# Optimization experiments

Hardware: AMD Instinct MI355X
Metric: run time of the kernel (lower is better)

Reference implementation:

```python
import jax, jax.numpy as jnp
import numpy as np
from jax import lax

R = 128            # grid resolution (full-depth N3Tree equivalent)
BASIS = 9          # SH degree 2 -> 9 basis functions
DATA_DIM = 3 * BASIS + 1
B = 262144         # rays (512x512 image)
STEP_SIZE = 0.001
BG = 1.0           # background_brightness
NUM_STEPS = 256    # >= sqrt(3)*R worst-case voxel crossings

SH_C0 = 0.28209479177387814
SH_C1 = 0.4886025119029199
SH_C2 = (1.0925484305920792, -1.0925484305920792, 0.31539156525252005,
         -1.0925484305920792, 0.5462742152960396)


def eval_sh_bases(d):
    # d: [B,3] unit view directions -> [B,9] SH deg-2 basis values (matches svox.sh)
    x, y, z = d[:, 0], d[:, 1], d[:, 2]
    return jnp.stack([
        jnp.full_like(x, SH_C0),
        -SH_C1 * y,
        SH_C1 * z,
        -SH_C1 * x,
        SH_C2[0] * x * y,
        SH_C2[1] * y * z,
        SH_C2[2] * (2.0 * z * z - x * x - y * y),
        SH_C2[3] * x * z,
        SH_C2[4] * (x * x - y * y),
    ], axis=-1)


def dda_unit(cen, invdir):
    # slab intersection of ray (cen + t*dir) with unit cube [0,1]^3
    t1 = -cen * invdir            # [B,3]
    t2 = t1 + invdir
    tmin = jnp.maximum(jnp.max(jnp.minimum(t1, t2), axis=-1), 0.0)
    tmax = jnp.minimum(jnp.min(jnp.maximum(t1, t2), axis=-1), 1e9)
    return tmin, tmax


def setup_inputs() -> dict:
    key = jax.random.key(0)
    k1, k2, k3, k4 = jax.random.split(key, 4)
    origins = jax.random.uniform(k1, (B, 3), jnp.float32, 0.05, 0.95)
    dirs = jax.random.normal(k2, (B, 3), jnp.float32)
    viewdirs = jax.random.normal(k3, (B, 3), jnp.float32)
    viewdirs = viewdirs / jnp.linalg.norm(viewdirs, axis=-1, keepdims=True)
    tree_data = jax.random.normal(k4, (R, R, R, DATA_DIM), jnp.float32) * 0.5
    invradius = jnp.ones((3,), jnp.float32)
    return {"tree_data": tree_data, "origins": origins, "dirs": dirs,
            "viewdirs": viewdirs, "invradius": invradius}


def _render(tree_data, origins, dirs, viewdirs, invradius):
    nb = origins.shape[0]
    dirs = dirs / jnp.linalg.norm(dirs, axis=-1, keepdims=True)
    sh_mult = eval_sh_bases(viewdirs)[:, None, :]          # [B,1,9]
    invdirs = 1.0 / (dirs + 1e-9)
    t0, tmax = dda_unit(origins, invdirs)
    delta_scale = jnp.linalg.norm(dirs / invradius[None], axis=-1)  # [B]
    grid = tree_data.reshape(R * R * R, DATA_DIM)
    cube_sz = 1.0 / R

    def step(carry, _):
        t, light, out, active = carry
        pos = origins + t[:, None] * dirs                  # [B,3] in tree coords
        idx = jnp.clip(jnp.floor(pos * R), 0.0, R - 1.0)
        flat = (idx[:, 0] * (R * R) + idx[:, 1] * R + idx[:, 2]).astype(jnp.int32)
        rgba = grid[flat]                                  # [B,28] voxel query
        pos_t = pos * R - idx                              # local coords in voxel
        s0, s1 = dda_unit(pos_t, invdirs)
        dt = (s1 - s0) * cube_sz + STEP_SIZE
        sigma = jax.nn.relu(rgba[:, -1])
        att = jnp.exp(-dt * sigma * delta_scale)
        weight = light * (1.0 - att)
        rgb_sh = rgba[:, :-1].reshape(-1, 3, BASIS)
        rgb = jax.nn.sigmoid(jnp.sum(sh_mult * rgb_sh, axis=-1))  # [B,3]
        am = active[:, None]
        out = out + jnp.where(am, weight[:, None] * rgb, 0.0)
        light = jnp.where(active, light * att, light)
        t = t + jnp.where(active, dt, 0.0)
        active = active & (t < tmax)
        return (t, light, out, active), None

    init = (t0, jnp.ones((nb,), jnp.float32), jnp.zeros((nb, 3), jnp.float32),
            t0 < tmax)
    (t, light, out, active), _ = lax.scan(step, init, None, length=NUM_STEPS)
    # remaining transmittance hits background (white by default)
    return out + light[:, None] * BG


def reference(tree_data, origins, dirs, viewdirs, invradius):
    return _render(tree_data, origins, dirs, viewdirs, invradius)
```

## Files before the change

### kernel.cpp

```cpp
#include <hip/hip_runtime.h>
#include <hip/hip_fp16.h>
#include <math.h>

#define GRID_R 128
#define DATA_DIM 28
#define PAD_DIM 32
#define NSEG 8
#define SEG_STEPS 32
#define STEP_SIZE 0.001f
#define BG 1.0f

typedef _Float16 h2f __attribute__((ext_vector_type(2)));

#if __has_builtin(__builtin_amdgcn_fdot2)
__device__ __forceinline__ float fdot2(h2f a, h2f b, float c) {
    return __builtin_amdgcn_fdot2(a, b, c, false);
}
#else
__device__ __forceinline__ float fdot2(h2f a, h2f b, float c) {
    return fmaf((float)a.x, (float)b.x, fmaf((float)a.y, (float)b.y, c));
}
#endif

#if __has_builtin(__builtin_amdgcn_exp2f)
__device__ __forceinline__ float fexp2(float x)    { return __builtin_amdgcn_exp2f(x); }
__device__ __forceinline__ float fexp2neg(float x) { return __builtin_amdgcn_exp2f(-x); }
#else
__device__ __forceinline__ float fexp2(float x) {
    float r; asm("v_exp_f32 %0, %1" : "=v"(r) : "v"(x)); return r;
}
__device__ __forceinline__ float fexp2neg(float x) {
    float r; asm("v_exp_f32 %0, -%1" : "=v"(r) : "v"(x)); return r;
}
#endif

#if __has_builtin(__builtin_amdgcn_rcpf)
__device__ __forceinline__ float frcp(float x) { return __builtin_amdgcn_rcpf(x); }
#else
__device__ __forceinline__ float frcp(float x) {
    float r; asm("v_rcp_f32 %0, %1" : "=v"(r) : "v"(x)); return r;
}
#endif

__device__ __forceinline__ float march_step(
    float t, float ox, float oy, float oz,
    float dx, float dy, float dz,
    float idx, float idy, float idz, int* flat)
{
    float px = (ox + t*dx) * 128.0f;
    float py = (oy + t*dy) * 128.0f;
    float pz = (oz + t*dz) * 128.0f;
    float fx = fminf(fmaxf(floorf(px), 0.0f), 127.0f);
    float fy = fminf(fmaxf(floorf(py), 0.0f), 127.0f);
    float fz = fminf(fmaxf(floorf(pz), 0.0f), 127.0f);
    float ff = fmaf(fx, 16384.0f, fmaf(fy, 128.0f, fz));
    *flat = (int)ff;
    float cx = px - fx, cy = py - fy, cz = pz - fz;
    float a1x = -cx*idx, a1y = -cy*idy, a1z = -cz*idz;
    float a2x = a1x+idx, a2y = a1y+idy, a2z = a1z+idz;
    float e1 = fminf(fminf(fmaxf(a1x,a2x), fmaxf(a1y,a2y)), fmaxf(a1z,a2z));
    e1 = fminf(e1, 1e9f);
    return e1 * (1.0f/128.0f) + STEP_SIZE;
}

#define RAY_SETUP(i)                                                          \
    float ox = origins[3*(i)+0], oy = origins[3*(i)+1], oz = origins[3*(i)+2];\
    float dx = dirs_in[3*(i)+0], dy = dirs_in[3*(i)+1], dz = dirs_in[3*(i)+2];\
    float dn = sqrtf(dx*dx + dy*dy + dz*dz);                                  \
    float rdn = 1.0f / dn;                                                    \
    dx *= rdn; dy *= rdn; dz *= rdn;                                          \
    float idx = 1.0f / (dx + 1e-9f);                                          \
    float idy = 1.0f / (dy + 1e-9f);                                          \
    float idz = 1.0f / (dz + 1e-9f);                                          \
    float t1x = -ox*idx, t1y = -oy*idy, t1z = -oz*idz;                        \
    float t2x = t1x+idx, t2y = t1y+idy, t2z = t1z+idz;                        \
    float t0   = fmaxf(fmaxf(fmaxf(fminf(t1x,t2x), fminf(t1y,t2y)), fminf(t1z,t2z)), 0.0f); \
    float tmax = fminf(fminf(fminf(fmaxf(t1x,t2x), fmaxf(t1y,t2y)), fmaxf(t1z,t2z)), 1e9f);

__global__ __launch_bounds__(256) void prep_kernel(
    const float* __restrict__ tree, __half* __restrict__ vox, int nvox,
    const float* __restrict__ origins, const float* __restrict__ dirs_in,
    float* __restrict__ ckpt, int nB, int nGeomB)
{
    if ((int)blockIdx.x < nGeomB) {
        int i = blockIdx.x * 256 + threadIdx.x;
        if (i >= nB) return;
        RAY_SETUP(i);
        float ck[NSEG];
        float t = t0;
        ck[0] = t0;
#pragma unroll
        for (int k = 1; k < NSEG; ++k) {
            if (t < tmax) {
                for (int j = 0; j < SEG_STEPS; ++j) {
                    int fl;
                    t += march_step(t, ox, oy, oz, dx, dy, dz, idx, idy, idz, &fl);
                    if (t >= tmax) break;
                }
            }
            ck[k] = t;
        }
        float* cp = ckpt + (size_t)i * NSEG;
        *(float4*)(cp + 0) = make_float4(ck[0], ck[1], ck[2], ck[3]);
        *(float4*)(cp + 4) = make_float4(ck[4], ck[5], ck[6], ck[7]);
    } else {
        int v = (blockIdx.x - nGeomB) * 256 + threadIdx.x;
        if (v >= nvox) return;
        const float4* s4 = (const float4*)(tree + (size_t)v * DATA_DIM);
        float4 A  = s4[0], B4 = s4[1], C4 = s4[2], D4 = s4[3],
               E4 = s4[4], F4 = s4[5], G4 = s4[6];
        uint4* d = (uint4*)(vox + (size_t)v * PAD_DIM);
        union Q { __half2 h[4]; uint4 u; } q;
        q.h[0] = __floats2half2_rn(A.x,  A.y);
        q.h[1] = __floats2half2_rn(A.z,  A.w);
        q.h[2] = __floats2half2_rn(B4.x, B4.y);
        q.h[3] = __floats2half2_rn(B4.z, B4.w);
        d[0] = q.u;
        q.h[0] = __floats2half2_rn(C4.x, 0.f);
        q.h[1] = __floats2half2_rn(C4.y, C4.z);
        q.h[2] = __floats2half2_rn(C4.w, D4.x);
        q.h[3] = __floats2half2_rn(D4.y, D4.z);
        d[1] = q.u;
        q.h[0] = __floats2half2_rn(D4.w, E4.x);
        q.h[1] = __floats2half2_rn(E4.y, 0.f);
        q.h[2] = __floats2half2_rn(E4.z, E4.w);
        q.h[3] = __floats2half2_rn(F4.x, F4.y);
        d[2] = q.u;
        q.h[0] = __floats2half2_rn(F4.z, F4.w);
        q.h[1] = __floats2half2_rn(G4.x, G4.y);
        q.h[2] = __floats2half2_rn(G4.z, 0.f);
        q.h[3] = __floats2half2_rn(G4.w, 0.f);
        d[3] = q.u;
    }
}

__global__ __launch_bounds__(256, 8) void march_kernel(
    const __half* __restrict__ vox_grid,
    const float* __restrict__ origins,
    const float* __restrict__ dirs_in,
    const float* __restrict__ viewdirs,
    const float* __restrict__ invradius,
    const float* __restrict__ ckpt,
    float* __restrict__ out, int nB)
{
    int tid = blockIdx.x * blockDim.x + threadIdx.x;
    int ray = tid >> 3;
    int seg = tid & 7;
    if (ray >= nB) return;

    RAY_SETUP(ray);

    float vx = viewdirs[3*ray+0], vy = viewdirs[3*ray+1], vz = viewdirs[3*ray+2];
    float irx = invradius[0], iry = invradius[1], irz = invradius[2];
    float qx = dx / irx, qy = dy / iry, qz = dz / irz;
    float delta_scale = sqrtf(qx*qx + qy*qy + qz*qz);

    const float C1 = 0.4886025119029199f;
    const float L2E = 1.4426950408889634f;
    float sh0 = 0.28209479177387814f;
    float sh1 = -C1 * vy;
    float sh2 =  C1 * vz;
    float sh3 = -C1 * vx;
    float sh4 =  1.0925484305920792f  * vx * vy;
    float sh5 = -1.0925484305920792f * vy * vz;
    float sh6 =  0.31539156525252005f * (2.0f*vz*vz - vx*vx - vy*vy);
    float sh7 = -1.0925484305920792f * vx * vz;
    float sh8 =  0.5462742152960396f  * (vx*vx - vy*vy);

    h2f S01 = { (_Float16)(sh0*L2E), (_Float16)(sh1*L2E) };
    h2f S23 = { (_Float16)(sh2*L2E), (_Float16)(sh3*L2E) };
    h2f S45 = { (_Float16)(sh4*L2E), (_Float16)(sh5*L2E) };
    h2f S67 = { (_Float16)(sh6*L2E), (_Float16)(sh7*L2E) };
    h2f S8z = { (_Float16)(sh8*L2E), (_Float16)0.0f      };
    float nds = -delta_scale * L2E;

    float t = ckpt[(size_t)ray * NSEG + seg];
    float light = 1.0f;
    float o0 = 0.f, o1 = 0.f, o2 = 0.f;

    for (int j = 0; j < SEG_STEPS; ++j) {
        if (t >= tmax) break;
        int flat;
        float dt = march_step(t, ox, oy, oz, dx, dy, dz, idx, idy, idz, &flat);

        const uint4* vp = (const uint4*)(vox_grid + (size_t)flat * PAD_DIM);
        union { uint4 u[4]; h2f h[16]; _Float16 s[32]; } rec;
        rec.u[0] = vp[0]; rec.u[1] = vp[1]; rec.u[2] = vp[2]; rec.u[3] = vp[3];

        float sigma = fmaxf((float)rec.s[30], 0.0f);
        float att = fexp2(dt * sigma * nds);
        float la  = light * att;
        float w   = light - la;
        light = la;

        float r0 = fdot2(rec.h[ 4], S8z, fdot2(rec.h[ 3], S67, fdot2(rec.h[ 2], S45,
                   fdot2(rec.h[ 1], S23, fdot2(rec.h[ 0], S01, 0.0f)))));
        float r1 = fdot2(rec.h[ 9], S8z, fdot2(rec.h[ 8], S67, fdot2(rec.h[ 7], S45,
                   fdot2(rec.h[ 6], S23, fdot2(rec.h[ 5], S01, 0.0f)))));
        float r2 = fdot2(rec.h[14], S8z, fdot2(rec.h[13], S67, fdot2(rec.h[12], S45,
                   fdot2(rec.h[11], S23, fdot2(rec.h[10], S01, 0.0f)))));

        float g0 = frcp(1.0f + fexp2neg(r0));
        float g1 = frcp(1.0f + fexp2neg(r1));
        float g2 = frcp(1.0f + fexp2neg(r2));

        o0 = fmaf(w, g0, o0);
        o1 = fmaf(w, g1, o1);
        o2 = fmaf(w, g2, o2);

        t += dt;
    }

    float l0 = __shfl(light, 0, 8);
    float l1 = __shfl(light, 1, 8);
    float l2 = __shfl(light, 2, 8);
    float l3 = __shfl(light, 3, 8);
    float l4 = __shfl(light, 4, 8);
    float l5 = __shfl(light, 5, 8);
    float l6 = __shfl(light, 6, 8);
    float l7 = __shfl(light, 7, 8);

    float P = 1.0f;
    if (seg > 0) P *= l0;
    if (seg > 1) P *= l1;
    if (seg > 2) P *= l2;
    if (seg > 3) P *= l3;
    if (seg > 4) P *= l4;
    if (seg > 5) P *= l5;
    if (seg > 6) P *= l6;
    float total_light = l0*l1*l2*l3*l4*l5*l6*l7;

    o0 *= P; o1 *= P; o2 *= P;
    o0 += __shfl_xor(o0, 1, 8); o0 += __shfl_xor(o0, 2, 8); o0 += __shfl_xor(o0, 4, 8);
    o1 += __shfl_xor(o1, 1, 8); o1 += __shfl_xor(o1, 2, 8); o1 += __shfl_xor(o1, 4, 8);
    o2 += __shfl_xor(o2, 1, 8); o2 += __shfl_xor(o2, 2, 8); o2 += __shfl_xor(o2, 4, 8);

    if (seg == 0) {
        out[3*ray+0] = o0 + total_light * BG;
        out[3*ray+1] = o1 + total_light * BG;
        out[3*ray+2] = o2 + total_light * BG;
    }
}

extern "C" void kernel_launch(void* const* d_in, const int* in_sizes, int n_in,
                              void* d_out, int out_size, void* d_ws, size_t ws_size,
                              hipStream_t stream) {
    const float* tree      = (const float*)d_in[0];
    const float* origins   = (const float*)d_in[1];
    const float* dirs      = (const float*)d_in[2];
    const float* viewdirs  = (const float*)d_in[3];
    const float* invradius = (const float*)d_in[4];
    float* out = (float*)d_out;

    int nB   = in_sizes[1] / 3;
    int nvox = in_sizes[0] / DATA_DIM;

    const int block = 256;
    __half* hgrid = (__half*)d_ws;
    float* ckpt = (float*)((char*)d_ws + (size_t)nvox * PAD_DIM * sizeof(__half));

    int nGeomB = (nB + block - 1) / block;
    int nConvB = (nvox + block - 1) / block;
    prep_kernel<<<nGeomB + nConvB, block, 0, stream>>>(
        tree, hgrid, nvox, origins, dirs, ckpt, nB, nGeomB);

    int nmarch = nB * NSEG;
    march_kernel<<<(nmarch + block - 1) / block, block, 0, stream>>>(
        hgrid, origins, dirs, viewdirs, invradius, ckpt, out, nB);
    (void)ws_size;
}
```

Before: 680.5 us.

## Software-pipeline voxel loads in march loop and split grid conversion across two threads

The march loop now computes the next step's voxel index and issues its 64-byte record load before shading the current voxel, double-buffering the two records so gather latency overlaps with SH and exp math. Separately, the fp32 to fp16 grid conversion uses two threads per voxel, each writing half of the padded record. The prefetch can load one extra voxel past the segment end and raises register pressure under launch bounds of 8 waves per SIMD. The conversion split doubles the thread count for that phase.

Result: slower. 706.4 us (+3.8%).

```diff
diff --git a/kernel.cpp b/kernel.cpp
--- a/kernel.cpp
+++ b/kernel.cpp
@@ -104,35 +104,72 @@
         *(float4*)(cp + 0) = make_float4(ck[0], ck[1], ck[2], ck[3]);
         *(float4*)(cp + 4) = make_float4(ck[4], ck[5], ck[6], ck[7]);
     } else {
-        int v = (blockIdx.x - nGeomB) * 256 + threadIdx.x;
+        int tid2 = (blockIdx.x - nGeomB) * 256 + threadIdx.x;
+        int v = tid2 >> 1;
+        int q = tid2 & 1;
         if (v >= nvox) return;
-        const float4* s4 = (const float4*)(tree + (size_t)v * DATA_DIM);
-        float4 A  = s4[0], B4 = s4[1], C4 = s4[2], D4 = s4[3],
-               E4 = s4[4], F4 = s4[5], G4 = s4[6];
-        uint4* d = (uint4*)(vox + (size_t)v * PAD_DIM);
-        union Q { __half2 h[4]; uint4 u; } q;
-        q.h[0] = __floats2half2_rn(A.x,  A.y);
-        q.h[1] = __floats2half2_rn(A.z,  A.w);
-        q.h[2] = __floats2half2_rn(B4.x, B4.y);
-        q.h[3] = __floats2half2_rn(B4.z, B4.w);
-        d[0] = q.u;
-        q.h[0] = __floats2half2_rn(C4.x, 0.f);
-        q.h[1] = __floats2half2_rn(C4.y, C4.z);
-        q.h[2] = __floats2half2_rn(C4.w, D4.x);
-        q.h[3] = __floats2half2_rn(D4.y, D4.z);
-        d[1] = q.u;
-        q.h[0] = __floats2half2_rn(D4.w, E4.x);
-        q.h[1] = __floats2half2_rn(E4.y, 0.f);
-        q.h[2] = __floats2half2_rn(E4.z, E4.w);
-        q.h[3] = __floats2half2_rn(F4.x, F4.y);
-        d[2] = q.u;
-        q.h[0] = __floats2half2_rn(F4.z, F4.w);
-        q.h[1] = __floats2half2_rn(G4.x, G4.y);
-        q.h[2] = __floats2half2_rn(G4.z, 0.f);
-        q.h[3] = __floats2half2_rn(G4.w, 0.f);
-        d[3] = q.u;
+        const float* src = tree + (size_t)v * DATA_DIM;
+        uint4* d = (uint4*)(vox + (size_t)v * PAD_DIM) + q * 2;
+        union Q { __half2 h[4]; uint4 u; } w;
+        if (q == 0) {
+            float4 L0 = *(const float4*)(src + 0);
+            float4 L1 = *(const float4*)(src + 4);
+            float4 L2 = *(const float4*)(src + 8);
+            float4 L3 = *(const float4*)(src + 12);
+            w.h[0] = __floats2half2_rn(L0.x, L0.y);
+            w.h[1] = __floats2half2_rn(L0.z, L0.w);
+            w.h[2] = __floats2half2_rn(L1.x, L1.y);
+            w.h[3] = __floats2half2_rn(L1.z, L1.w);
+            d[0] = w.u;
+            w.h[0] = __floats2half2_rn(L2.x, 0.f);
+            w.h[1] = __floats2half2_rn(L2.y, L2.z);
+            w.h[2] = __floats2half2_rn(L2.w, L3.x);
+            w.h[3] = __floats2half2_rn(L3.y, L3.z);
+            d[1] = w.u;
+        } else {
+            float4 M0 = *(const float4*)(src + 12);
+            float4 M1 = *(const float4*)(src + 16);
+            float4 M2 = *(const float4*)(src + 20);
+            float4 M3 = *(const float4*)(src + 24);
+            w.h[0] = __floats2half2_rn(M0.w, M1.x);
+            w.h[1] = __floats2half2_rn(M1.y, 0.f);
+            w.h[2] = __floats2half2_rn(M1.z, M1.w);
+            w.h[3] = __floats2half2_rn(M2.x, M2.y);
+            d[0] = w.u;
+            w.h[0] = __floats2half2_rn(M2.z, M2.w);
+            w.h[1] = __floats2half2_rn(M3.x, M3.y);
+            w.h[2] = __floats2half2_rn(M3.z, 0.f);
+            w.h[3] = __floats2half2_rn(M3.w, 0.f);
+            d[1] = w.u;
+        }
     }
 }
+
+typedef union { uint4 u[4]; h2f h[16]; _Float16 s[32]; } Rec;
+
+#define LOADREC(R, FLAT) do {                                                 \
+    const uint4* _vp = (const uint4*)(vox_grid + (size_t)(FLAT) * PAD_DIM);   \
+    (R).u[0] = _vp[0]; (R).u[1] = _vp[1];                                     \
+    (R).u[2] = _vp[2]; (R).u[3] = _vp[3]; } while (0)
+
+#define SHADE(R, DT) do {                                                     \
+    float _sig = fmaxf((float)(R).s[30], 0.0f);                               \
+    float _att = fexp2((DT) * _sig * nds);                                    \
+    float _la  = light * _att;                                                \
+    float _w   = light - _la;                                                 \
+    light = _la;                                                              \
+    float _r0 = fdot2((R).h[ 4], S8z, fdot2((R).h[ 3], S67, fdot2((R).h[ 2], S45, \
+                fdot2((R).h[ 1], S23, fdot2((R).h[ 0], S01, 0.0f)))));        \
+    float _r1 = fdot2((R).h[ 9], S8z, fdot2((R).h[ 8], S67, fdot2((R).h[ 7], S45, \
+                fdot2((R).h[ 6], S23, fdot2((R).h[ 5], S01, 0.0f)))));        \
+    float _r2 = fdot2((R).h[14], S8z, fdot2((R).h[13], S67, fdot2((R).h[12], S45, \
+                fdot2((R).h[11], S23, fdot2((R).h[10], S01, 0.0f)))));        \
+    float _g0 = frcp(1.0f + fexp2neg(_r0));                                   \
+    float _g1 = frcp(1.0f + fexp2neg(_r1));                                   \
+    float _g2 = frcp(1.0f + fexp2neg(_r2));                                   \
+    o0 = fmaf(_w, _g0, o0);                                                   \
+    o1 = fmaf(_w, _g1, o1);                                                   \
+    o2 = fmaf(_w, _g2, o2); } while (0)
 
 __global__ __launch_bounds__(256, 8) void march_kernel(
     const __half* __restrict__ vox_grid,
@@ -178,37 +215,25 @@
     float light = 1.0f;
     float o0 = 0.f, o1 = 0.f, o2 = 0.f;
 
-    for (int j = 0; j < SEG_STEPS; ++j) {
-        if (t >= tmax) break;
-        int flat;
-        float dt = march_step(t, ox, oy, oz, dx, dy, dz, idx, idy, idz, &flat);
-
-        const uint4* vp = (const uint4*)(vox_grid + (size_t)flat * PAD_DIM);
-        union { uint4 u[4]; h2f h[16]; _Float16 s[32]; } rec;
-        rec.u[0] = vp[0]; rec.u[1] = vp[1]; rec.u[2] = vp[2]; rec.u[3] = vp[3];
-
-        float sigma = fmaxf((float)rec.s[30], 0.0f);
-        float att = fexp2(dt * sigma * nds);
-        float la  = light * att;
-        float w   = light - la;
-        light = la;
-
-        float r0 = fdot2(rec.h[ 4], S8z, fdot2(rec.h[ 3], S67, fdot2(rec.h[ 2], S45,
-                   fdot2(rec.h[ 1], S23, fdot2(rec.h[ 0], S01, 0.0f)))));
-        float r1 = fdot2(rec.h[ 9], S8z, fdot2(rec.h[ 8], S67, fdot2(rec.h[ 7], S45,
-                   fdot2(rec.h[ 6], S23, fdot2(rec.h[ 5], S01, 0.0f)))));
-        float r2 = fdot2(rec.h[14], S8z, fdot2(rec.h[13], S67, fdot2(rec.h[12], S45,
-                   fdot2(rec.h[11], S23, fdot2(rec.h[10], S01, 0.0f)))));
-
-        float g0 = frcp(1.0f + fexp2neg(r0));
-        float g1 = frcp(1.0f + fexp2neg(r1));
-        float g2 = frcp(1.0f + fexp2neg(r2));
-
-        o0 = fmaf(w, g0, o0);
-        o1 = fmaf(w, g1, o1);
-        o2 = fmaf(w, g2, o2);
-
-        t += dt;
+    if (t < tmax) {
+        int fA, fB;
+        Rec A, B;
+        float dtA = march_step(t, ox, oy, oz, dx, dy, dz, idx, idy, idz, &fA);
+        LOADREC(A, fA);
+        int i = 0;
+        for (;;) {
+            t += dtA;
+            float dtB = march_step(t, ox, oy, oz, dx, dy, dz, idx, idy, idz, &fB);
+            LOADREC(B, fB);
+            SHADE(A, dtA);
+            if (++i >= SEG_STEPS || t >= tmax) break;
+
+            t += dtB;
+            dtA = march_step(t, ox, oy, oz, dx, dy, dz, idx, idy, idz, &fA);
+            LOADREC(A, fA);
+            SHADE(B, dtB);
+            if (++i >= SEG_STEPS || t >= tmax) break;
+        }
     }
 
     float l0 = __shfl(light, 0, 8);
@@ -260,7 +285,7 @@
     float* ckpt = (float*)((char*)d_ws + (size_t)nvox * PAD_DIM * sizeof(__half));
 
     int nGeomB = (nB + block - 1) / block;
-    int nConvB = (nvox + block - 1) / block;
+    int nConvB = (nvox * 2 + block - 1) / block;
     prep_kernel<<<nGeomB + nConvB, block, 0, stream>>>(
         tree, hgrid, nvox, origins, dirs, ckpt, nB, nGeomB);
 
```
